# Kernel optimization log

Hardware: AMD Instinct MI355X
Metric: run time of the kernel (lower is better)

## Reference

```python
import jax, jax.numpy as jnp
import numpy as np

B, HGT, WID, D, NS = 4, 64, 128, 128, 2
LN_EPS = 1e-5

def layer_norm(x, g, b):
    m = jnp.mean(x, axis=-1, keepdims=True)
    v = jnp.mean((x - m) ** 2, axis=-1, keepdims=True)
    return (x - m) * jax.lax.rsqrt(v + LN_EPS) * g + b

def setup_inputs() -> dict:
    key = jax.random.key(0)
    ks = jax.random.split(key, 8)
    src = jax.random.normal(ks[0], (B, HGT * WID, D), jnp.float32)
    L = (HGT // NS) * (WID // NS)  # 2048
    s = 0.05
    return {
        "source": src,
        "target": src,  # identical -> self-attention branch in original
        "shifted_window_attn_mask": jax.random.normal(ks[1], (NS * NS, L, L), jnp.float32),
        "shifted_window_attn_mask_1d": jnp.zeros((NS, WID // NS, WID // NS), jnp.float32),
        "height": HGT,
        "width": WID,
        "attn_num_splits": NS,
        "with_shift": 1,
        "Wq": jax.random.normal(ks[2], (D, D), jnp.float32) * s,
        "Wk": jax.random.normal(ks[3], (D, D), jnp.float32) * s,
        "Wv": jax.random.normal(ks[4], (D, D), jnp.float32) * s,
        "Wm": jax.random.normal(ks[5], (D, D), jnp.float32) * s,
        "g1": jnp.ones((D,), jnp.float32),
        "b1": jnp.zeros((D,), jnp.float32),
        "W1": jax.random.normal(ks[6], (2 * D, 8 * D), jnp.float32) * s,
        "W2": jax.random.normal(ks[7], (8 * D, D), jnp.float32) * s,
        "g2": jnp.ones((D,), jnp.float32),
        "b2": jnp.zeros((D,), jnp.float32),
    }

def _shifted_window_self_attn(q, k, v, ns, with_shift, h, w, attn_mask):
    b, _, c = q.shape
    hh, ww = h // ns, w // ns  # window sizes
    sh, sw = hh // 2, ww // 2
    L = hh * ww

    def to_windows(x):
        x = x.reshape(b, h, w, c)
        if with_shift:
            x = jnp.roll(x, shift=(-sh, -sw), axis=(1, 2))
        # (b, ns, hh, ns, ww, c) -> (b*ns*ns, hh*ww, c)
        x = x.reshape(b, ns, hh, ns, ww, c).transpose(0, 1, 3, 2, 4, 5)
        return x.reshape(b * ns * ns, L, c)

    qw, kw, vw = to_windows(q), to_windows(k), to_windows(v)
    scores = jnp.einsum("bqc,bkc->bqk", qw, kw) / (c ** 0.5)  # (b*ns^2, L, L)
    if with_shift:
        scores = (scores.reshape(b, ns * ns, L, L) + attn_mask).reshape(b * ns * ns, L, L)
    attn = jax.nn.softmax(scores, axis=-1)
    out = jnp.einsum("bqk,bkc->bqc", attn, vw)
    # merge windows back
    out = out.reshape(b, ns, ns, hh, ww, c).transpose(0, 1, 3, 2, 4, 5).reshape(b, h, w, c)
    if with_shift:
        out = jnp.roll(out, shift=(sh, sw), axis=(1, 2))
    return out.reshape(b, h * w, c)

def reference(source, target, shifted_window_attn_mask, shifted_window_attn_mask_1d,
              height, width, attn_num_splits, with_shift,
              Wq, Wk, Wv, Wm, g1, b1, W1, W2, g2, b2):
    # target == source -> self-attention, attn_num_splits > 1 -> shifted-window path
    q = source @ Wq
    k = target @ Wk
    v = target @ Wv
    message = _shifted_window_self_attn(q, k, v, attn_num_splits, with_shift,
                                        height, width, shifted_window_attn_mask)
    message = layer_norm(message @ Wm, g1, b1)
    h = jnp.concatenate([source, message], axis=-1)  # (B, HW, 2D)
    message = jax.nn.gelu(h @ W1, approximate=False) @ W2
    message = layer_norm(message, g2, b2)
    return source + message
```

## Files before the change

kernel.cpp:

```cpp
#include <hip/hip_runtime.h>

typedef unsigned short u16;
typedef __bf16 bf16x8 __attribute__((ext_vector_type(8)));
typedef float f32x4 __attribute__((ext_vector_type(4)));

#define MFMA(a, b, c) __builtin_amdgcn_mfma_f32_16x16x32_bf16(a, b, c, 0, 0, 0)


__device__ __forceinline__ u16 f2b(float f) {
  unsigned u = __builtin_bit_cast(unsigned, f);
  u += 0x7fffu + ((u >> 16) & 1u);
  return (u16)(u >> 16);
}
__device__ __forceinline__ float b2f(u16 h) {
  unsigned u = (unsigned)h << 16;
  return __builtin_bit_cast(float, u);
}
__device__ __forceinline__ void glds16(const u16* g, u16* l) {
  __builtin_amdgcn_global_load_lds((const __attribute__((address_space(1))) void*)g,
                                   (__attribute__((address_space(3))) void*)l, 16, 0, 0);
}

#define QW_OFF   ((size_t)0)
#define KW_OFF   ((size_t)8 << 20)
#define VBUF_OFF ((size_t)16 << 20)
#define O1_OFF   ((size_t)24 << 20)
#define O2_OFF   ((size_t)40 << 20)
#define SRCB_OFF ((size_t)64 << 20)
#define MSG1_OFF ((size_t)72 << 20)
#define L1_OFF   ((size_t)80 << 20)
#define L2P_OFF  (((size_t)80 << 20) + 131072)
#define WQT_OFF  (((size_t)80 << 20) + 262144)
#define WKT_OFF  (WQT_OFF + 32768)
#define WVT_OFF  (WQT_OFF + 65536)
#define WMT_OFF  (WQT_OFF + 98304)
#define W1T_OFF  (WQT_OFF + 131072)
#define W2T_OFF  (WQT_OFF + 655360)

__global__ void k_prep(const float* __restrict__ wq, const float* __restrict__ wk,
                       const float* __restrict__ wv, const float* __restrict__ wm,
                       const float* __restrict__ w1, const float* __restrict__ w2,
                       u16* __restrict__ wqt, u16* __restrict__ wkt,
                       u16* __restrict__ wvt, u16* __restrict__ wmt,
                       u16* __restrict__ w1t, u16* __restrict__ w2t) {
  int t = blockIdx.x * 256 + threadIdx.x;
  if (t < 65536) {
    int m = t >> 14, loc = t & 16383;
    int n = loc >> 7, k = loc & 127;
    const float* s = (m == 0) ? wq : (m == 1) ? wk : (m == 2) ? wv : wm;
    u16* d = (m == 0) ? wqt : (m == 1) ? wkt : (m == 2) ? wvt : wmt;
    const float sc = (m == 0) ? 0.08838834764831845f : 1.0f;
    d[n * 128 + k] = f2b(s[k * 128 + n] * sc);
  } else if (t < 65536 + 262144) {
    int loc = t - 65536;
    int n = loc >> 8, k = loc & 255;
    w1t[n * 256 + k] = f2b(w1[k * 1024 + n]);
  } else if (t < 65536 + 262144 + 131072) {
    int loc = t - 327680;
    int n = loc >> 10, k = loc & 1023;
    w2t[n * 1024 + k] = f2b(w2[k * 128 + n]);
  }
}

__global__ __launch_bounds__(256, 2)
void k_qkv(const float* __restrict__ src,
           const u16* __restrict__ wtq, const u16* __restrict__ wtk,
           const u16* __restrict__ wtv,
           u16* __restrict__ qw, u16* __restrict__ kw, u16* __restrict__ vbuf,
           u16* __restrict__ srcb) {
  __shared__ __align__(16) u16 At[64 * 136];
  __shared__ __align__(16) u16 Bt[128 * 136];
  const int tid = threadIdx.x, bid = blockIdx.x;
  const int lane = tid & 63, wid = tid >> 6;
  const int l15 = lane & 15, quad = lane >> 4;

  {
    const int row = tid >> 2, part = tid & 3;
    const int t = bid * 64 + row;
    const int g = t >> 11, p = t & 2047;
    const int b = g >> 2, wi = (g >> 1) & 1, wj = g & 1;
    const int ii = p >> 6, jj = p & 63;
    const int y = (wi * 32 + ii + 16) & 63;
    const int x = (wj * 64 + jj + 32) & 127;
    const int srow = b * 8192 + y * 128 + x;
    const float4* sp = (const float4*)(src + srow * 128) + part * 8;
    u16* lp = &At[row * 136 + part * 32];
    u16* gp = srcb + srow * 128 + part * 32;
#pragma unroll
    for (int q = 0; q < 8; ++q) {
      float4 v = sp[q];
      ushort4 h = make_ushort4(f2b(v.x), f2b(v.y), f2b(v.z), f2b(v.w));
      *(ushort4*)(lp + q * 4) = h;
      *(ushort4*)(gp + q * 4) = h;
    }
  }
  __syncthreads();

  bf16x8 afrag[4];
  const int arow = wid * 16 + l15;
#pragma unroll
  for (int kk = 0; kk < 4; ++kk)
    afrag[kk] = *(const bf16x8*)&At[arow * 136 + kk * 32 + quad * 8];

  const f32x4 fz = {0.f, 0.f, 0.f, 0.f};
#pragma unroll 1
  for (int m = 0; m < 3; ++m) {
    const u16* wp = (m == 0) ? wtq : (m == 1) ? wtk : wtv;
    {
      const int n = tid >> 1, half = tid & 1;
      const uint4* sp = (const uint4*)(wp + n * 128 + half * 64);
      uint4* dp = (uint4*)&Bt[n * 136 + half * 64];
#pragma unroll
      for (int q = 0; q < 8; ++q) dp[q] = sp[q];
    }
    __syncthreads();
    f32x4 acc[8];
#pragma unroll
    for (int nt = 0; nt < 8; ++nt) acc[nt] = fz;
#pragma unroll
    for (int kk = 0; kk < 4; ++kk) {
#pragma unroll
      for (int nt = 0; nt < 8; ++nt) {
        bf16x8 bfr = *(const bf16x8*)&Bt[(nt * 16 + l15) * 136 + kk * 32 + quad * 8];
        acc[nt] = MFMA(afrag[kk], bfr, acc[nt]);
      }
    }
    const int t0 = bid * 64 + wid * 16 + quad * 4;
    if (m < 2) {
      u16* dst = (m == 0) ? qw : kw;
#pragma unroll
      for (int nt = 0; nt < 8; ++nt) {
        const int d = nt * 16 + l15;
#pragma unroll
        for (int r = 0; r < 4; ++r) dst[(t0 + r) * 128 + d] = f2b(acc[nt][r]);
      }
    } else {
      const int g = bid >> 5;
      const int p0 = t0 & 2047;
#pragma unroll
      for (int nt = 0; nt < 8; ++nt) {
        const int d = nt * 16 + l15;
        ushort4 hv = make_ushort4(f2b(acc[nt][0]), f2b(acc[nt][1]),
                                  f2b(acc[nt][2]), f2b(acc[nt][3]));
        *(ushort4*)&vbuf[g * 262144 + d * 2048 + p0] = hv;
      }
    }
    __syncthreads();
  }
}

__global__ __launch_bounds__(256, 2)
void k_attn(const u16* __restrict__ qw, const u16* __restrict__ kw,
            const u16* __restrict__ vbuf, const float* __restrict__ mask,
            u16* __restrict__ o1, u16* __restrict__ o2,
            float* __restrict__ l1, float* __restrict__ l2) {
  __shared__ __align__(16) u16 Kt[2][64 * 128];
  __shared__ __align__(16) u16 Vt[2][128 * 64];
  __shared__ __align__(16) u16 Pt[128 * 40];
  const int tid = threadIdx.x;
  const int bid = (blockIdx.x & 7) * 64 + (blockIdx.x >> 3);
  const int lane = tid & 63, wid = tid >> 6;
  const int l15 = lane & 15, quad = lane >> 4;
  const int b = bid & 3, w = (bid >> 2) & 3, half = (bid >> 4) & 1, qb = bid >> 5;
  const int g = b * 4 + w;
  const int k0 = half * 1024;
  const u16* kbase = kw + g * 262144 + k0 * 128;
  const u16* vbase = vbuf + g * 262144 + k0;
  const int qrow0 = qb * 128 + wid * 32;
  const float* mlane = mask + (size_t)w * 4194304 + (size_t)(qrow0 + quad * 4) * 2048 + k0 + l15;

  int offk[4], offv[4], dstb[4];
#pragma unroll
  for (int j = 0; j < 4; ++j) {
    const int s = wid * 256 + j * 64 + lane;
    const int rk = s >> 4, bk = (s & 15) ^ (rk & 15);
    offk[j] = rk * 128 + bk * 8;
    const int dv = s >> 3, bv = (s & 7) ^ (dv & 7);
    offv[j] = dv * 2048 + bv * 8;
    dstb[j] = (wid * 256 + j * 64) * 8;
  }

  bf16x8 qfrag[2][4];
#pragma unroll
  for (int qs = 0; qs < 2; ++qs) {
    const u16* qp = qw + g * 262144 + (qrow0 + qs * 16 + l15) * 128 + quad * 8;
#pragma unroll
    for (int kk = 0; kk < 4; ++kk) qfrag[qs][kk] = *(const bf16x8*)(qp + kk * 32);
  }
  const f32x4 fz = {0.f, 0.f, 0.f, 0.f};
  f32x4 o[2][8];
#pragma unroll
  for (int qs = 0; qs < 2; ++qs)
#pragma unroll
    for (int nt = 0; nt < 8; ++nt) o[qs][nt] = fz;
  float lr[2][4] = {{0.f, 0.f, 0.f, 0.f}, {0.f, 0.f, 0.f, 0.f}};
  const float L2E = 1.4426950408889634f;

#pragma unroll
  for (int j = 0; j < 4; ++j) {
    glds16(kbase + offk[j], &Kt[0][dstb[j]]);
    glds16(vbase + offv[j], &Vt[0][dstb[j]]);
  }
  float mpf[16];
#pragma unroll
  for (int qs = 0; qs < 2; ++qs)
#pragma unroll
    for (int ntl = 0; ntl < 2; ++ntl)
#pragma unroll
      for (int r = 0; r < 4; ++r)
        mpf[qs * 8 + ntl * 4 + r] = mlane[(qs * 16 + r) * 2048 + ntl * 16];

#pragma unroll 1
  for (int kt = 0; kt < 16; ++kt) {
    const int p = kt & 1;
    __syncthreads();
    if (kt < 15) {
      const u16* kb = kbase + (kt + 1) * 8192;
      const u16* vb = vbase + (kt + 1) * 64;
#pragma unroll
      for (int j = 0; j < 4; ++j) {
        glds16(kb + offk[j], &Kt[p ^ 1][dstb[j]]);
        glds16(vb + offv[j], &Vt[p ^ 1][dstb[j]]);
      }
    }
#pragma unroll
    for (int ks = 0; ks < 2; ++ks) {
      float mn[16];
      const bool hasn = (kt < 15) || (ks == 0);
      const int ncol = kt * 64 + 32 + ks * 32;
      if (hasn) {
#pragma unroll
        for (int qs = 0; qs < 2; ++qs)
#pragma unroll
          for (int ntl = 0; ntl < 2; ++ntl)
#pragma unroll
            for (int r = 0; r < 4; ++r)
              mn[qs * 8 + ntl * 4 + r] = mlane[(qs * 16 + r) * 2048 + ncol + ntl * 16];
      }
      f32x4 s[2][2];
#pragma unroll
      for (int qs = 0; qs < 2; ++qs)
#pragma unroll
        for (int ntl = 0; ntl < 2; ++ntl)
#pragma unroll
          for (int r = 0; r < 4; ++r) s[qs][ntl][r] = mpf[qs * 8 + ntl * 4 + r];
#pragma unroll
      for (int kk = 0; kk < 4; ++kk)
#pragma unroll
        for (int ntl = 0; ntl < 2; ++ntl) {
          bf16x8 kfr = *(const bf16x8*)&Kt[p][(ks * 32 + ntl * 16 + l15) * 128 +
                                             (((kk * 4 + quad) ^ l15) * 8)];
          s[0][ntl] = MFMA(qfrag[0][kk], kfr, s[0][ntl]);
          s[1][ntl] = MFMA(qfrag[1][kk], kfr, s[1][ntl]);
        }
#pragma unroll
      for (int qs = 0; qs < 2; ++qs)
#pragma unroll
        for (int ntl = 0; ntl < 2; ++ntl)
#pragma unroll
          for (int r = 0; r < 4; ++r) {
            const float pv = exp2f(s[qs][ntl][r] * L2E);
            lr[qs][r] += pv;
            Pt[(wid * 32 + qs * 16 + quad * 4 + r) * 40 + ntl * 16 + l15] = f2b(pv);
          }
      bf16x8 pf0 = *(const bf16x8*)&Pt[(wid * 32 + l15) * 40 + quad * 8];
      bf16x8 pf1 = *(const bf16x8*)&Pt[(wid * 32 + 16 + l15) * 40 + quad * 8];
#pragma unroll
      for (int nt = 0; nt < 8; ++nt) {
        bf16x8 vfr = *(const bf16x8*)&Vt[p][(nt * 16 + l15) * 64 +
                                            (((ks * 4 + quad) ^ (l15 & 7)) * 8)];
        o[0][nt] = MFMA(pf0, vfr, o[0][nt]);
        o[1][nt] = MFMA(pf1, vfr, o[1][nt]);
      }
      if (hasn) {
#pragma unroll
        for (int i = 0; i < 16; ++i) mpf[i] = mn[i];
      }
    }
  }

#pragma unroll
  for (int off = 1; off < 16; off <<= 1)
#pragma unroll
    for (int qs = 0; qs < 2; ++qs)
#pragma unroll
      for (int r = 0; r < 4; ++r) lr[qs][r] += __shfl_xor(lr[qs][r], off, 16);
  u16* op = half ? o2 : o1;
  float* lp = half ? l2 : l1;
#pragma unroll
  for (int qs = 0; qs < 2; ++qs) {
    const int t0 = g * 2048 + qrow0 + qs * 16 + quad * 4;
#pragma unroll
    for (int r = 0; r < 4; ++r) {
      const float inv = 1.f / lr[qs][r];
#pragma unroll
      for (int nt = 0; nt < 8; ++nt)
        op[(size_t)(t0 + r) * 128 + nt * 16 + l15] = f2b(o[qs][nt][r] * inv);
      if (l15 == 0) lp[t0 + r] = lr[qs][r];
    }
  }
}

__global__ __launch_bounds__(256, 2)
void k_wmln(const u16* __restrict__ o1, const u16* __restrict__ o2,
            const float* __restrict__ l1, const float* __restrict__ l2,
            const u16* __restrict__ wmt, const float* __restrict__ g1,
            const float* __restrict__ b1, u16* __restrict__ msg1) {
  __shared__ __align__(16) u16 At[64 * 136];
  __shared__ __align__(16) u16 Bt[128 * 136];
  const int tid = threadIdx.x, bid = blockIdx.x;
  const int lane = tid & 63, wid = tid >> 6;
  const int l15 = lane & 15, quad = lane >> 4;
  {
    const int row = tid >> 2, part = tid & 3;
    const int m = bid * 64 + row;
    const float la = l1[m], lb = l2[m];
    const float wA = la / (la + lb), wB = lb / (la + lb);
    const u16* p1 = o1 + (size_t)m * 128 + part * 32;
    const u16* p2 = o2 + (size_t)m * 128 + part * 32;
    u16* lp = &At[row * 136 + part * 32];
#pragma unroll
    for (int q = 0; q < 4; ++q) {
      ushort4 xa = *(const ushort4*)(p1 + q * 8);
      ushort4 xb = *(const ushort4*)(p1 + q * 8 + 4);
      ushort4 ya = *(const ushort4*)(p2 + q * 8);
      ushort4 yb = *(const ushort4*)(p2 + q * 8 + 4);
      ushort4 ha = make_ushort4(f2b(b2f(xa.x) * wA + b2f(ya.x) * wB),
                                f2b(b2f(xa.y) * wA + b2f(ya.y) * wB),
                                f2b(b2f(xa.z) * wA + b2f(ya.z) * wB),
                                f2b(b2f(xa.w) * wA + b2f(ya.w) * wB));
      ushort4 hb = make_ushort4(f2b(b2f(xb.x) * wA + b2f(yb.x) * wB),
                                f2b(b2f(xb.y) * wA + b2f(yb.y) * wB),
                                f2b(b2f(xb.z) * wA + b2f(yb.z) * wB),
                                f2b(b2f(xb.w) * wA + b2f(yb.w) * wB));
      *(ushort4*)(lp + q * 8) = ha;
      *(ushort4*)(lp + q * 8 + 4) = hb;
    }
  }
  {
    const int n = tid >> 1, half = tid & 1;
    const uint4* sp = (const uint4*)(wmt + n * 128 + half * 64);
    uint4* dp = (uint4*)&Bt[n * 136 + half * 64];
#pragma unroll
    for (int q = 0; q < 8; ++q) dp[q] = sp[q];
  }
  __syncthreads();
  bf16x8 afrag[4];
  const int arow = wid * 16 + l15;
#pragma unroll
  for (int kk = 0; kk < 4; ++kk)
    afrag[kk] = *(const bf16x8*)&At[arow * 136 + kk * 32 + quad * 8];
  const f32x4 fz = {0.f, 0.f, 0.f, 0.f};
  f32x4 acc[8];
#pragma unroll
  for (int nt = 0; nt < 8; ++nt) acc[nt] = fz;
#pragma unroll
  for (int kk = 0; kk < 4; ++kk)
#pragma unroll
    for (int nt = 0; nt < 8; ++nt) {
      bf16x8 bfr = *(const bf16x8*)&Bt[(nt * 16 + l15) * 136 + kk * 32 + quad * 8];
      acc[nt] = MFMA(afrag[kk], bfr, acc[nt]);
    }
  float sum[4] = {0, 0, 0, 0}, sq[4] = {0, 0, 0, 0};
#pragma unroll
  for (int nt = 0; nt < 8; ++nt)
#pragma unroll
    for (int r = 0; r < 4; ++r) {
      const float v = acc[nt][r];
      sum[r] += v;
      sq[r] += v * v;
    }
#pragma unroll
  for (int off = 1; off < 16; off <<= 1)
#pragma unroll
    for (int r = 0; r < 4; ++r) {
      sum[r] += __shfl_xor(sum[r], off, 16);
      sq[r] += __shfl_xor(sq[r], off, 16);
    }
  float mean[4], rstd[4];
#pragma unroll
  for (int r = 0; r < 4; ++r) {
    mean[r] = sum[r] * (1.f / 128.f);
    const float var = sq[r] * (1.f / 128.f) - mean[r] * mean[r];
    rstd[r] = rsqrtf(var + 1e-5f);
  }
  const int t0 = bid * 64 + wid * 16 + quad * 4;
#pragma unroll
  for (int nt = 0; nt < 8; ++nt) {
    const int d = nt * 16 + l15;
    const float gg = g1[d], bb = b1[d];
#pragma unroll
    for (int r = 0; r < 4; ++r) {
      const int tt = t0 + r;
      msg1[(size_t)tt * 128 + d] = f2b((acc[nt][r] - mean[r]) * rstd[r] * gg + bb);
    }
  }
}

__global__ __launch_bounds__(256, 2)
void k_mlp(const u16* __restrict__ srcb, const u16* __restrict__ msg1,
           const u16* __restrict__ w1t, const u16* __restrict__ w2t,
           const float* __restrict__ g2, const float* __restrict__ b2,
           const float* __restrict__ src, float* __restrict__ out) {
  __shared__ __align__(16) u16 Bt1[64 * 256];
  __shared__ __align__(16) u16 Bt2[128 * 64];
  __shared__ __align__(16) u16 Ht[128 * 72];
  const int tid = threadIdx.x, bid = blockIdx.x;
  const int lane = tid & 63, wid = tid >> 6;
  const int l15 = lane & 15, quad = lane >> 4;

  int off1[8], db1[8], off2[4], db2[4];
#pragma unroll
  for (int j = 0; j < 8; ++j) {
    const int s = wid * 512 + j * 64 + lane;
    const int r = s >> 5, c = s & 31;
    off1[j] = r * 256 + (c ^ (r & 15)) * 8;
    db1[j] = (wid * 512 + j * 64) * 8;
  }
#pragma unroll
  for (int j = 0; j < 4; ++j) {
    const int s = wid * 256 + j * 64 + lane;
    const int r = s >> 3, c = s & 7;
    off2[j] = r * 1024 + (c ^ (r & 7)) * 8;
    db2[j] = (wid * 256 + j * 64) * 8;
  }

  bf16x8 afrag[2][8];
#pragma unroll
  for (int qs = 0; qs < 2; ++qs) {
    const int t_sp = bid * 128 + qs * 64 + wid * 16 + l15;
    const u16* sp = srcb + (size_t)t_sp * 128 + quad * 8;
    const int bb = t_sp >> 13, rem = t_sp & 8191;
    const int y = rem >> 7, x = rem & 127;
    const int u = (y + 48) & 63, v = (x + 96) & 127;
    const int wrow = (bb * 4 + (u >> 5) * 2 + (v >> 6)) * 2048 + (u & 31) * 64 + (v & 63);
    const u16* mp = msg1 + (size_t)wrow * 128 + quad * 8;
#pragma unroll
    for (int kk = 0; kk < 4; ++kk) {
      afrag[qs][kk] = *(const bf16x8*)(sp + kk * 32);
      afrag[qs][kk + 4] = *(const bf16x8*)(mp + kk * 32);
    }
  }
  const f32x4 fz = {0.f, 0.f, 0.f, 0.f};
  f32x4 oacc[2][8];
#pragma unroll
  for (int qs = 0; qs < 2; ++qs)
#pragma unroll
    for (int nt = 0; nt < 8; ++nt) oacc[qs][nt] = fz;

#pragma unroll 1
  for (int hc = 0; hc < 16; ++hc) {
    __syncthreads();
#pragma unroll
    for (int j = 0; j < 8; ++j) glds16(w1t + hc * 16384 + off1[j], &Bt1[db1[j]]);
#pragma unroll
    for (int j = 0; j < 4; ++j) glds16(w2t + hc * 64 + off2[j], &Bt2[db2[j]]);
    __syncthreads();

    f32x4 hacc[2][4];
#pragma unroll
    for (int qs = 0; qs < 2; ++qs)
#pragma unroll
      for (int nt = 0; nt < 4; ++nt) hacc[qs][nt] = fz;
#pragma unroll
    for (int kk = 0; kk < 8; ++kk)
#pragma unroll
      for (int nt = 0; nt < 4; ++nt) {
        bf16x8 b1 = *(const bf16x8*)&Bt1[(nt * 16 + l15) * 256 +
                                         (((kk * 4 + quad) ^ l15) * 8)];
        hacc[0][nt] = MFMA(afrag[0][kk], b1, hacc[0][nt]);
        hacc[1][nt] = MFMA(afrag[1][kk], b1, hacc[1][nt]);
      }
#pragma unroll
    for (int qs = 0; qs < 2; ++qs)
#pragma unroll
      for (int nt = 0; nt < 4; ++nt)
#pragma unroll
        for (int r = 0; r < 4; ++r) {
          const float x = hacc[qs][nt][r];
          const float y = 0.5f * x * (1.f + erff(x * 0.70710678118654752f));
          Ht[(qs * 64 + wid * 16 + quad * 4 + r) * 72 + nt * 16 + l15] = f2b(y);
        }
    bf16x8 hf[2][2];
#pragma unroll
    for (int qs = 0; qs < 2; ++qs) {
      hf[qs][0] = *(const bf16x8*)&Ht[(qs * 64 + wid * 16 + l15) * 72 + quad * 8];
      hf[qs][1] = *(const bf16x8*)&Ht[(qs * 64 + wid * 16 + l15) * 72 + 32 + quad * 8];
    }
#pragma unroll
    for (int kk2 = 0; kk2 < 2; ++kk2)
#pragma unroll
      for (int nt = 0; nt < 8; ++nt) {
        bf16x8 b2fr = *(const bf16x8*)&Bt2[(nt * 16 + l15) * 64 +
                                           (((kk2 * 4 + quad) ^ (l15 & 7)) * 8)];
        oacc[0][nt] = MFMA(hf[0][kk2], b2fr, oacc[0][nt]);
        oacc[1][nt] = MFMA(hf[1][kk2], b2fr, oacc[1][nt]);
      }
  }

#pragma unroll
  for (int qs = 0; qs < 2; ++qs) {
    float sum[4] = {0, 0, 0, 0}, sq[4] = {0, 0, 0, 0};
#pragma unroll
    for (int nt = 0; nt < 8; ++nt)
#pragma unroll
      for (int r = 0; r < 4; ++r) {
        const float v = oacc[qs][nt][r];
        sum[r] += v;
        sq[r] += v * v;
      }
#pragma unroll
    for (int off = 1; off < 16; off <<= 1)
#pragma unroll
      for (int r = 0; r < 4; ++r) {
        sum[r] += __shfl_xor(sum[r], off, 16);
        sq[r] += __shfl_xor(sq[r], off, 16);
      }
    float mean[4], rstd[4];
#pragma unroll
    for (int r = 0; r < 4; ++r) {
      mean[r] = sum[r] * (1.f / 128.f);
      const float var = sq[r] * (1.f / 128.f) - mean[r] * mean[r];
      rstd[r] = rsqrtf(var + 1e-5f);
    }
    const int t0 = bid * 128 + qs * 64 + wid * 16 + quad * 4;
#pragma unroll
    for (int nt = 0; nt < 8; ++nt) {
      const int d = nt * 16 + l15;
      const float gg = g2[d], bb = b2[d];
#pragma unroll
      for (int r = 0; r < 4; ++r) {
        const int idx = (t0 + r) * 128 + d;
        out[idx] = src[idx] + (oacc[qs][nt][r] - mean[r]) * rstd[r] * gg + bb;
      }
    }
  }
}

extern "C" void kernel_launch(void* const* d_in, const int* in_sizes, int n_in,
                              void* d_out, int out_size, void* d_ws, size_t ws_size,
                              hipStream_t stream) {
  const float* src  = (const float*)d_in[0];
  const float* mask = (const float*)d_in[2];
  const float* Wq = (const float*)d_in[8];
  const float* Wk = (const float*)d_in[9];
  const float* Wv = (const float*)d_in[10];
  const float* Wm = (const float*)d_in[11];
  const float* g1 = (const float*)d_in[12];
  const float* b1 = (const float*)d_in[13];
  const float* W1 = (const float*)d_in[14];
  const float* W2 = (const float*)d_in[15];
  const float* g2 = (const float*)d_in[16];
  const float* b2 = (const float*)d_in[17];
  char* ws = (char*)d_ws;
  u16* qw   = (u16*)(ws + QW_OFF);
  u16* kw   = (u16*)(ws + KW_OFF);
  u16* vbuf = (u16*)(ws + VBUF_OFF);
  u16* o1   = (u16*)(ws + O1_OFF);
  u16* o2   = (u16*)(ws + O2_OFF);
  float* l1 = (float*)(ws + L1_OFF);
  float* l2 = (float*)(ws + L2P_OFF);
  u16* srcb = (u16*)(ws + SRCB_OFF);
  u16* msg1 = (u16*)(ws + MSG1_OFF);
  u16* wqt = (u16*)(ws + WQT_OFF);
  u16* wkt = (u16*)(ws + WKT_OFF);
  u16* wvt = (u16*)(ws + WVT_OFF);
  u16* wmt = (u16*)(ws + WMT_OFF);
  u16* w1t = (u16*)(ws + W1T_OFF);
  u16* w2t = (u16*)(ws + W2T_OFF);

  k_prep<<<1792, 256, 0, stream>>>(Wq, Wk, Wv, Wm, W1, W2, wqt, wkt, wvt, wmt, w1t, w2t);
  k_qkv<<<512, 256, 0, stream>>>(src, wqt, wkt, wvt, qw, kw, vbuf, srcb);
  k_attn<<<512, 256, 0, stream>>>(qw, kw, vbuf, mask, o1, o2, l1, l2);
  k_wmln<<<512, 256, 0, stream>>>(o1, o2, l1, l2, wmt, g1, b1, msg1);
  k_mlp<<<256, 256, 0, stream>>>(srcb, msg1, w1t, w2t, g2, b2, src, (float*)d_out);
}
```

Measured before the change: 315.7 us.

## Double-buffer MLP weight tiles and halve tokens per block

```diff
diff --git a/kernel.cpp b/kernel.cpp
--- a/kernel.cpp
+++ b/kernel.cpp
@@ -402,33 +402,32 @@
            const u16* __restrict__ w1t, const u16* __restrict__ w2t,
            const float* __restrict__ g2, const float* __restrict__ b2,
            const float* __restrict__ src, float* __restrict__ out) {
-  __shared__ __align__(16) u16 Bt1[64 * 256];
-  __shared__ __align__(16) u16 Bt2[128 * 64];
-  __shared__ __align__(16) u16 Ht[128 * 72];
+  __shared__ __align__(16) u16 Bt1[2][32 * 256];
+  __shared__ __align__(16) u16 Bt2[2][128 * 32];
+  __shared__ __align__(16) u16 Ht[64 * 40];
   const int tid = threadIdx.x, bid = blockIdx.x;
   const int lane = tid & 63, wid = tid >> 6;
   const int l15 = lane & 15, quad = lane >> 4;
 
-  int off1[8], db1[8], off2[4], db2[4];
-#pragma unroll
-  for (int j = 0; j < 8; ++j) {
-    const int s = wid * 512 + j * 64 + lane;
+  int off1[4], db1[4], off2[2], db2[2];
+#pragma unroll
+  for (int j = 0; j < 4; ++j) {
+    const int s = wid * 256 + j * 64 + lane;
     const int r = s >> 5, c = s & 31;
     off1[j] = r * 256 + (c ^ (r & 15)) * 8;
-    db1[j] = (wid * 512 + j * 64) * 8;
-  }
-#pragma unroll
-  for (int j = 0; j < 4; ++j) {
-    const int s = wid * 256 + j * 64 + lane;
-    const int r = s >> 3, c = s & 7;
-    off2[j] = r * 1024 + (c ^ (r & 7)) * 8;
-    db2[j] = (wid * 256 + j * 64) * 8;
-  }
-
-  bf16x8 afrag[2][8];
-#pragma unroll
-  for (int qs = 0; qs < 2; ++qs) {
-    const int t_sp = bid * 128 + qs * 64 + wid * 16 + l15;
+    db1[j] = (wid * 256 + j * 64) * 8;
+  }
+#pragma unroll
+  for (int j = 0; j < 2; ++j) {
+    const int s = wid * 128 + j * 64 + lane;
+    const int r = s >> 2, c = s & 3;
+    off2[j] = r * 1024 + (c ^ (r & 3)) * 8;
+    db2[j] = (wid * 128 + j * 64) * 8;
+  }
+
+  bf16x8 afrag[8];
+  {
+    const int t_sp = bid * 64 + wid * 16 + l15;
     const u16* sp = srcb + (size_t)t_sp * 128 + quad * 8;
     const int bb = t_sp >> 13, rem = t_sp & 8191;
     const int y = rem >> 7, x = rem & 127;
@@ -437,102 +436,93 @@
     const u16* mp = msg1 + (size_t)wrow * 128 + quad * 8;
 #pragma unroll
     for (int kk = 0; kk < 4; ++kk) {
-      afrag[qs][kk] = *(const bf16x8*)(sp + kk * 32);
-      afrag[qs][kk + 4] = *(const bf16x8*)(mp + kk * 32);
+      afrag[kk] = *(const bf16x8*)(sp + kk * 32);
+      afrag[kk + 4] = *(const bf16x8*)(mp + kk * 32);
     }
   }
   const f32x4 fz = {0.f, 0.f, 0.f, 0.f};
-  f32x4 oacc[2][8];
-#pragma unroll
-  for (int qs = 0; qs < 2; ++qs)
-#pragma unroll
-    for (int nt = 0; nt < 8; ++nt) oacc[qs][nt] = fz;
+  f32x4 oacc[8];
+#pragma unroll
+  for (int nt = 0; nt < 8; ++nt) oacc[nt] = fz;
+
+#pragma unroll
+  for (int j = 0; j < 4; ++j) glds16(w1t + off1[j], &Bt1[0][db1[j]]);
+#pragma unroll
+  for (int j = 0; j < 2; ++j) glds16(w2t + off2[j], &Bt2[0][db2[j]]);
 
 #pragma unroll 1
-  for (int hc = 0; hc < 16; ++hc) {
+  for (int hc = 0; hc < 32; ++hc) {
+    const int p = hc & 1;
     __syncthreads();
-#pragma unroll
-    for (int j = 0; j < 8; ++j) glds16(w1t + hc * 16384 + off1[j], &Bt1[db1[j]]);
-#pragma unroll
-    for (int j = 0; j < 4; ++j) glds16(w2t + hc * 64 + off2[j], &Bt2[db2[j]]);
-    __syncthreads();
-
-    f32x4 hacc[2][4];
-#pragma unroll
-    for (int qs = 0; qs < 2; ++qs)
-#pragma unroll
-      for (int nt = 0; nt < 4; ++nt) hacc[qs][nt] = fz;
+    if (hc < 31) {
+#pragma unroll
+      for (int j = 0; j < 4; ++j)
+        glds16(w1t + (hc + 1) * 8192 + off1[j], &Bt1[p ^ 1][db1[j]]);
+#pragma unroll
+      for (int j = 0; j < 2; ++j)
+        glds16(w2t + (hc + 1) * 32 + off2[j], &Bt2[p ^ 1][db2[j]]);
+    }
+
+    f32x4 hacc[2];
+    hacc[0] = fz;
+    hacc[1] = fz;
 #pragma unroll
     for (int kk = 0; kk < 8; ++kk)
 #pragma unroll
-      for (int nt = 0; nt < 4; ++nt) {
-        bf16x8 b1 = *(const bf16x8*)&Bt1[(nt * 16 + l15) * 256 +
-                                         (((kk * 4 + quad) ^ l15) * 8)];
-        hacc[0][nt] = MFMA(afrag[0][kk], b1, hacc[0][nt]);
-        hacc[1][nt] = MFMA(afrag[1][kk], b1, hacc[1][nt]);
-      }
-#pragma unroll
-    for (int qs = 0; qs < 2; ++qs)
-#pragma unroll
-      for (int nt = 0; nt < 4; ++nt)
-#pragma unroll
-        for (int r = 0; r < 4; ++r) {
-          const float x = hacc[qs][nt][r];
-          const float y = 0.5f * x * (1.f + erff(x * 0.70710678118654752f));
-          Ht[(qs * 64 + wid * 16 + quad * 4 + r) * 72 + nt * 16 + l15] = f2b(y);
-        }
-    bf16x8 hf[2][2];
-#pragma unroll
-    for (int qs = 0; qs < 2; ++qs) {
-      hf[qs][0] = *(const bf16x8*)&Ht[(qs * 64 + wid * 16 + l15) * 72 + quad * 8];
-      hf[qs][1] = *(const bf16x8*)&Ht[(qs * 64 + wid * 16 + l15) * 72 + 32 + quad * 8];
-    }
-#pragma unroll
-    for (int kk2 = 0; kk2 < 2; ++kk2)
-#pragma unroll
-      for (int nt = 0; nt < 8; ++nt) {
-        bf16x8 b2fr = *(const bf16x8*)&Bt2[(nt * 16 + l15) * 64 +
-                                           (((kk2 * 4 + quad) ^ (l15 & 7)) * 8)];
-        oacc[0][nt] = MFMA(hf[0][kk2], b2fr, oacc[0][nt]);
-        oacc[1][nt] = MFMA(hf[1][kk2], b2fr, oacc[1][nt]);
-      }
-  }
-
-#pragma unroll
-  for (int qs = 0; qs < 2; ++qs) {
-    float sum[4] = {0, 0, 0, 0}, sq[4] = {0, 0, 0, 0};
-#pragma unroll
-    for (int nt = 0; nt < 8; ++nt)
+      for (int nt = 0; nt < 2; ++nt) {
+        bf16x8 b1fr = *(const bf16x8*)&Bt1[p][(nt * 16 + l15) * 256 +
+                                             (((kk * 4 + quad) ^ l15) * 8)];
+        hacc[nt] = MFMA(afrag[kk], b1fr, hacc[nt]);
+      }
+#pragma unroll
+    for (int nt = 0; nt < 2; ++nt)
 #pragma unroll
       for (int r = 0; r < 4; ++r) {
-        const float v = oacc[qs][nt][r];
-        sum[r] += v;
-        sq[r] += v * v;
-      }
-#pragma unroll
-    for (int off = 1; off < 16; off <<= 1)
-#pragma unroll
-      for (int r = 0; r < 4; ++r) {
-        sum[r] += __shfl_xor(sum[r], off, 16);
-        sq[r] += __shfl_xor(sq[r], off, 16);
-      }
-    float mean[4], rstd[4];
-#pragma unroll
-    for (int r = 0; r < 4; ++r) {
-      mean[r] = sum[r] * (1.f / 128.f);
-      const float var = sq[r] * (1.f / 128.f) - mean[r] * mean[r];
-      rstd[r] = rsqrtf(var + 1e-5f);
-    }
-    const int t0 = bid * 128 + qs * 64 + wid * 16 + quad * 4;
+        const float x = hacc[nt][r];
+        const float y = 0.5f * x * (1.f + erff(x * 0.70710678118654752f));
+        Ht[(wid * 16 + quad * 4 + r) * 40 + nt * 16 + l15] = f2b(y);
+      }
+    bf16x8 hf = *(const bf16x8*)&Ht[(wid * 16 + l15) * 40 + quad * 8];
 #pragma unroll
     for (int nt = 0; nt < 8; ++nt) {
-      const int d = nt * 16 + l15;
-      const float gg = g2[d], bb = b2[d];
-#pragma unroll
-      for (int r = 0; r < 4; ++r) {
-        const int idx = (t0 + r) * 128 + d;
-        out[idx] = src[idx] + (oacc[qs][nt][r] - mean[r]) * rstd[r] * gg + bb;
-      }
+      bf16x8 b2fr = *(const bf16x8*)&Bt2[p][(nt * 16 + l15) * 32 +
+                                           ((quad ^ (l15 & 3)) * 8)];
+      oacc[nt] = MFMA(hf, b2fr, oacc[nt]);
+    }
+  }
+
+  float sum[4] = {0, 0, 0, 0}, sq[4] = {0, 0, 0, 0};
+#pragma unroll
+  for (int nt = 0; nt < 8; ++nt)
+#pragma unroll
+    for (int r = 0; r < 4; ++r) {
+      const float v = oacc[nt][r];
+      sum[r] += v;
+      sq[r] += v * v;
+    }
+#pragma unroll
+  for (int off = 1; off < 16; off <<= 1)
+#pragma unroll
+    for (int r = 0; r < 4; ++r) {
+      sum[r] += __shfl_xor(sum[r], off, 16);
+      sq[r] += __shfl_xor(sq[r], off, 16);
+    }
+  float mean[4], rstd[4];
+#pragma unroll
+  for (int r = 0; r < 4; ++r) {
+    mean[r] = sum[r] * (1.f / 128.f);
+    const float var = sq[r] * (1.f / 128.f) - mean[r] * mean[r];
+    rstd[r] = rsqrtf(var + 1e-5f);
+  }
+  const int t0 = bid * 64 + wid * 16 + quad * 4;
+#pragma unroll
+  for (int nt = 0; nt < 8; ++nt) {
+    const int d = nt * 16 + l15;
+    const float gg = g2[d], bb = b2[d];
+#pragma unroll
+    for (int r = 0; r < 4; ++r) {
+      const int idx = (t0 + r) * 128 + d;
+      out[idx] = src[idx] + (oacc[nt][r] - mean[r]) * rstd[r] * gg + bb;
     }
   }
 }
@@ -573,5 +563,5 @@
   k_qkv<<<512, 256, 0, stream>>>(src, wqt, wkt, wvt, qw, kw, vbuf, srcb);
   k_attn<<<512, 256, 0, stream>>>(qw, kw, vbuf, mask, o1, o2, l1, l2);
   k_wmln<<<512, 256, 0, stream>>>(o1, o2, l1, l2, wmt, g1, b1, msg1);
-  k_mlp<<<256, 256, 0, stream>>>(srcb, msg1, w1t, w2t, g2, b2, src, (float*)d_out);
-}
+  k_mlp<<<512, 256, 0, stream>>>(srcb, msg1, w1t, w2t, g2, b2, src, (float*)d_out);
+}
```

Result: faster. 295.6 us (-6.4%).
